# Performance work log

Measured on AMD Instinct MI355X. Metric: run time of the kernel, lower is better.

Reference implementation:

```python
import jax, jax.numpy as jnp
import numpy as np


def setup_inputs() -> dict:
    key = jax.random.key(0)
    k1, k2 = jax.random.split(key)
    B, C, T = 64, 16, 32768
    y_pred = jax.random.normal(k1, (B, C, T), dtype=jnp.float32)
    y_true = jax.random.normal(k2, (B, C, T), dtype=jnp.float32)
    return {"y_pred": y_pred, "y_true": y_true}


def reference(y_pred, y_true):
    # Original: for i in 1..T, sum |cumsum(pred[:,:,:i]) - cumsum(true[:,:,:i])|, mean over batch.
    # Prefix position t (0-indexed) appears in all outer iterations i >= t+1, i.e. (T - t) times.
    # => total = mean_b sum_{c,t} |cumsum(pred - true)[b,c,t]| * (T - t)
    B, C, T = y_pred.shape
    c = jnp.cumsum(y_pred - y_true, axis=2)          # (B, C, T)
    w = (T - jnp.arange(T)).astype(y_pred.dtype)     # weight T-t for position t
    total = jnp.sum(jnp.abs(c) * w, axis=(1, 2))     # (B,)
    total = jnp.mean(total)
    scaling = 2.0 / (T * C * (T * C + 1))            # apply_scaling_factor=True
    return scaling * total
```

## Files before the change

kernel.cpp:

```cpp
#include <hip/hip_runtime.h>

#define B_BATCH 64
#define C_CH    16
#define T_LEN   32768
#define THREADS 256
#define VEC     4
#define CHUNK   (THREADS * VEC)
#define NCHUNK  (T_LEN / CHUNK)
#define CPP     8
#define NPH     (NCHUNK / CPP)
#define PHEL    (CPP * CHUNK)
#define NROWS   (B_BATCH * C_CH)

__global__ __launch_bounds__(THREADS, 4) void wloss_scan_kernel(
    const float* __restrict__ pred,
    const float* __restrict__ tru,
    double* __restrict__ partials)
{
    __shared__ float  s_pref[PHEL];
    __shared__ float  s_wt[CPP * 4];
    __shared__ float  s_rowc;
    __shared__ double s_d[4];

    const int row  = blockIdx.x;
    const int tid  = threadIdx.x;
    const int lane = tid & 63;
    const int wave = tid >> 6;

    const float4* p4 = (const float4*)(pred + (size_t)row * T_LEN);
    const float4* t4 = (const float4*)(tru  + (size_t)row * T_LEN);

    if (tid == 0) s_rowc = 0.0f;
    double acc = 0.0;

    for (int ph = 0; ph < NPH; ++ph) {
        if (ph) __syncthreads();

        #pragma unroll
        for (int c8 = 0; c8 < CPP; ++c8) {
            const int c   = ph * CPP + c8;
            const int idx = c * (CHUNK / VEC) + tid;
            float4 p = p4[idx];
            float4 t = t4[idx];
            float d0 = p.x - t.x, d1 = p.y - t.y, d2 = p.z - t.z, d3 = p.w - t.w;
            float s1 = d0, s2 = s1 + d1, s3 = s2 + d2, s4 = s3 + d3;

            float v = s4;
            #pragma unroll
            for (int off = 1; off < 64; off <<= 1) {
                float u = __shfl_up(v, off, 64);
                if (lane >= off) v += u;
            }
            const float we = v - s4;
            float4 st = { we + s1, we + s2, we + s3, we + s4 };
            *(float4*)&s_pref[c8 * CHUNK + tid * VEC] = st;
            if (lane == 63) s_wt[c8 * 4 + wave] = v;
        }
        __syncthreads();

        if (wave == 0) {
            float val = (lane < 32) ? s_wt[lane] : 0.0f;
            float inc = val;
            #pragma unroll
            for (int off = 1; off < 32; off <<= 1) {
                float u = __shfl_up(inc, off, 64);
                if (lane >= off) inc += u;
            }
            const float rc = s_rowc;
            if (lane < 32) s_wt[lane] = rc + inc - val;
            if (lane == 31) s_rowc = rc + inc;
        }
        __syncthreads();

        #pragma unroll
        for (int c8 = 0; c8 < CPP; ++c8) {
            const float carry = s_wt[c8 * 4 + wave];
            float4 pr = *(const float4*)&s_pref[c8 * CHUNK + tid * VEC];
            const int   e0 = (ph * CPP + c8) * CHUNK + tid * VEC;
            const float w0 = (float)(T_LEN - e0);
            float part = fabsf(carry + pr.x) * w0
                       + fabsf(carry + pr.y) * (w0 - 1.0f)
                       + fabsf(carry + pr.z) * (w0 - 2.0f)
                       + fabsf(carry + pr.w) * (w0 - 3.0f);
            acc += (double)part;
        }
    }

    #pragma unroll
    for (int off = 32; off > 0; off >>= 1)
        acc += __shfl_down(acc, off, 64);
    if (lane == 0) s_d[wave] = acc;
    __syncthreads();

    if (tid == 0)
        partials[row] = s_d[0] + s_d[1] + s_d[2] + s_d[3];
}

__global__ __launch_bounds__(THREADS) void wloss_finalize_kernel(
    const double* __restrict__ partials, float* __restrict__ out)
{
    const int tid  = threadIdx.x;
    const int lane = tid & 63;
    const int wave = tid >> 6;

    double acc = 0.0;
    for (int i = tid; i < NROWS; i += THREADS) acc += partials[i];

    #pragma unroll
    for (int off = 32; off > 0; off >>= 1)
        acc += __shfl_down(acc, off, 64);

    __shared__ double dtot[4];
    if (lane == 0) dtot[wave] = acc;
    __syncthreads();

    if (tid == 0) {
        const double tot     = dtot[0] + dtot[1] + dtot[2] + dtot[3];
        const double tc      = (double)T_LEN * (double)C_CH;
        const double scaling = 2.0 / (tc * (tc + 1.0));
        out[0] = (float)(tot * scaling / (double)B_BATCH);
    }
}

extern "C" void kernel_launch(void* const* d_in, const int* in_sizes, int n_in,
                              void* d_out, int out_size, void* d_ws, size_t ws_size,
                              hipStream_t stream)
{
    const float* pred = (const float*)d_in[0];
    const float* tru  = (const float*)d_in[1];
    double*      partials = (double*)d_ws;
    float*       out      = (float*)d_out;

    wloss_scan_kernel<<<NROWS, THREADS, 0, stream>>>(pred, tru, partials);
    wloss_finalize_kernel<<<1, THREADS, 0, stream>>>(partials, out);
}
```

Baseline: 279.8 us.

## Split row scan into tile-sum and weighted-scan kernels for more parallelism

Replaces the one-block-per-row sequential chunk scan with a reduce-then-scan scheme. A first kernel computes per-tile sums of pred-true across 16 tiles per row. A second kernel computes each tile's carry from the preceding tile sums and does a local scan and weighted abs-sum. This raises the block count from 1024 to 16384 and removes the LDS-staged phases, at the cost of reading both inputs twice and adding a kernel launch.

```diff
diff --git a/kernel.cpp b/kernel.cpp
--- a/kernel.cpp
+++ b/kernel.cpp
@@ -4,96 +4,110 @@
 #define C_CH    16
 #define T_LEN   32768
 #define THREADS 256
-#define VEC     4
-#define CHUNK   (THREADS * VEC)
-#define NCHUNK  (T_LEN / CHUNK)
-#define CPP     8
-#define NPH     (NCHUNK / CPP)
-#define PHEL    (CPP * CHUNK)
+#define TPT     8
+#define TILE    (THREADS * TPT)
+#define NTILE   (T_LEN / TILE)
 #define NROWS   (B_BATCH * C_CH)
+#define NBLK    (NROWS * NTILE)
 
-__global__ __launch_bounds__(THREADS, 4) void wloss_scan_kernel(
+#define TS_OFF   0
+#define PART_OFF (NBLK * 4)
+
+__global__ __launch_bounds__(THREADS, 8) void wloss_sum_kernel(
     const float* __restrict__ pred,
     const float* __restrict__ tru,
-    double* __restrict__ partials)
+    float* __restrict__ tilesum)
 {
-    __shared__ float  s_pref[PHEL];
-    __shared__ float  s_wt[CPP * 4];
-    __shared__ float  s_rowc;
-    __shared__ double s_d[4];
-
-    const int row  = blockIdx.x;
     const int tid  = threadIdx.x;
     const int lane = tid & 63;
     const int wave = tid >> 6;
+    const int row  = blockIdx.x >> 4;
+    const int g    = blockIdx.x & (NTILE - 1);
 
-    const float4* p4 = (const float4*)(pred + (size_t)row * T_LEN);
-    const float4* t4 = (const float4*)(tru  + (size_t)row * T_LEN);
+    const size_t base = (size_t)row * T_LEN + (size_t)g * TILE;
+    const float4* p4 = (const float4*)(pred + base) + tid * 2;
+    const float4* t4 = (const float4*)(tru  + base) + tid * 2;
 
-    if (tid == 0) s_rowc = 0.0f;
-    double acc = 0.0;
+    float4 a0 = p4[0], a1 = p4[1];
+    float4 b0 = t4[0], b1 = t4[1];
 
-    for (int ph = 0; ph < NPH; ++ph) {
-        if (ph) __syncthreads();
-
-        #pragma unroll
-        for (int c8 = 0; c8 < CPP; ++c8) {
-            const int c   = ph * CPP + c8;
-            const int idx = c * (CHUNK / VEC) + tid;
-            float4 p = p4[idx];
-            float4 t = t4[idx];
-            float d0 = p.x - t.x, d1 = p.y - t.y, d2 = p.z - t.z, d3 = p.w - t.w;
-            float s1 = d0, s2 = s1 + d1, s3 = s2 + d2, s4 = s3 + d3;
-
-            float v = s4;
-            #pragma unroll
-            for (int off = 1; off < 64; off <<= 1) {
-                float u = __shfl_up(v, off, 64);
-                if (lane >= off) v += u;
-            }
-            const float we = v - s4;
-            float4 st = { we + s1, we + s2, we + s3, we + s4 };
-            *(float4*)&s_pref[c8 * CHUNK + tid * VEC] = st;
-            if (lane == 63) s_wt[c8 * 4 + wave] = v;
-        }
-        __syncthreads();
-
-        if (wave == 0) {
-            float val = (lane < 32) ? s_wt[lane] : 0.0f;
-            float inc = val;
-            #pragma unroll
-            for (int off = 1; off < 32; off <<= 1) {
-                float u = __shfl_up(inc, off, 64);
-                if (lane >= off) inc += u;
-            }
-            const float rc = s_rowc;
-            if (lane < 32) s_wt[lane] = rc + inc - val;
-            if (lane == 31) s_rowc = rc + inc;
-        }
-        __syncthreads();
-
-        #pragma unroll
-        for (int c8 = 0; c8 < CPP; ++c8) {
-            const float carry = s_wt[c8 * 4 + wave];
-            float4 pr = *(const float4*)&s_pref[c8 * CHUNK + tid * VEC];
-            const int   e0 = (ph * CPP + c8) * CHUNK + tid * VEC;
-            const float w0 = (float)(T_LEN - e0);
-            float part = fabsf(carry + pr.x) * w0
-                       + fabsf(carry + pr.y) * (w0 - 1.0f)
-                       + fabsf(carry + pr.z) * (w0 - 2.0f)
-                       + fabsf(carry + pr.w) * (w0 - 3.0f);
-            acc += (double)part;
-        }
-    }
+    float s = (a0.x - b0.x) + (a0.y - b0.y) + (a0.z - b0.z) + (a0.w - b0.w)
+            + (a1.x - b1.x) + (a1.y - b1.y) + (a1.z - b1.z) + (a1.w - b1.w);
 
     #pragma unroll
     for (int off = 32; off > 0; off >>= 1)
+        s += __shfl_down(s, off, 64);
+
+    __shared__ float s_w[4];
+    if (lane == 0) s_w[wave] = s;
+    __syncthreads();
+    if (tid == 0)
+        tilesum[blockIdx.x] = s_w[0] + s_w[1] + s_w[2] + s_w[3];
+}
+
+__global__ __launch_bounds__(THREADS, 8) void wloss_weight_kernel(
+    const float* __restrict__ pred,
+    const float* __restrict__ tru,
+    const float* __restrict__ tilesum,
+    double* __restrict__ partials)
+{
+    const int tid  = threadIdx.x;
+    const int lane = tid & 63;
+    const int wave = tid >> 6;
+    const int row  = blockIdx.x >> 4;
+    const int g    = blockIdx.x & (NTILE - 1);
+
+    const size_t base = (size_t)row * T_LEN + (size_t)g * TILE;
+    const float4* p4 = (const float4*)(pred + base) + tid * 2;
+    const float4* t4 = (const float4*)(tru  + base) + tid * 2;
+
+    float4 a0 = p4[0], a1 = p4[1];
+    float4 b0 = t4[0], b1 = t4[1];
+
+    float carry = 0.0f;
+    for (int j = 0; j < g; ++j)
+        carry += tilesum[(row << 4) + j];
+
+    float d[TPT];
+    d[0] = a0.x - b0.x; d[1] = a0.y - b0.y; d[2] = a0.z - b0.z; d[3] = a0.w - b0.w;
+    d[4] = a1.x - b1.x; d[5] = a1.y - b1.y; d[6] = a1.z - b1.z; d[7] = a1.w - b1.w;
+    #pragma unroll
+    for (int j = 1; j < TPT; ++j) d[j] += d[j-1];
+
+    float v = d[TPT-1];
+    #pragma unroll
+    for (int off = 1; off < 64; off <<= 1) {
+        float u = __shfl_up(v, off, 64);
+        if (lane >= off) v += u;
+    }
+    const float texcl = v - d[TPT-1];
+
+    __shared__ float s_w[4];
+    if (lane == 63) s_w[wave] = v;
+    __syncthreads();
+    float wprefix = 0.0f;
+    #pragma unroll
+    for (int w = 0; w < 4; ++w)
+        if (w < wave) wprefix += s_w[w];
+
+    const float excl = carry + wprefix + texcl;
+    const int   e0   = g * TILE + tid * TPT;
+    const float w0   = (float)(T_LEN - e0);
+    float part = 0.0f;
+    #pragma unroll
+    for (int j = 0; j < TPT; ++j)
+        part += fabsf(excl + d[j]) * (w0 - (float)j);
+
+    double acc = (double)part;
+    #pragma unroll
+    for (int off = 32; off > 0; off >>= 1)
         acc += __shfl_down(acc, off, 64);
+
+    __shared__ double s_d[4];
     if (lane == 0) s_d[wave] = acc;
     __syncthreads();
-
     if (tid == 0)
-        partials[row] = s_d[0] + s_d[1] + s_d[2] + s_d[3];
+        partials[blockIdx.x] = s_d[0] + s_d[1] + s_d[2] + s_d[3];
 }
 
 __global__ __launch_bounds__(THREADS) void wloss_finalize_kernel(
@@ -104,7 +118,7 @@
     const int wave = tid >> 6;
 
     double acc = 0.0;
-    for (int i = tid; i < NROWS; i += THREADS) acc += partials[i];
+    for (int i = tid; i < NBLK; i += THREADS) acc += partials[i];
 
     #pragma unroll
     for (int off = 32; off > 0; off >>= 1)
@@ -128,9 +142,11 @@
 {
     const float* pred = (const float*)d_in[0];
     const float* tru  = (const float*)d_in[1];
-    double*      partials = (double*)d_ws;
-    float*       out      = (float*)d_out;
+    float*  tilesum  = (float*) ((char*)d_ws + TS_OFF);
+    double* partials = (double*)((char*)d_ws + PART_OFF);
+    float*  out      = (float*)d_out;
 
-    wloss_scan_kernel<<<NROWS, THREADS, 0, stream>>>(pred, tru, partials);
-    wloss_finalize_kernel<<<1, THREADS, 0, stream>>>(partials, out);
+    wloss_sum_kernel     <<<NBLK, THREADS, 0, stream>>>(pred, tru, tilesum);
+    wloss_weight_kernel  <<<NBLK, THREADS, 0, stream>>>(pred, tru, tilesum, partials);
+    wloss_finalize_kernel<<<1,    THREADS, 0, stream>>>(partials, out);
 }
```

Result: slower. 322.4 us (+15.2%).

## Replace phased LDS prefix buffering with per-chunk register scan and prefetch

Applied to the files above, without the earlier changes.

The scan kernel no longer buffers eight chunks of prefixes in shared memory. Each chunk is now scanned in registers, with a double-buffered per-wave total array and a redundant cross-wave prefix computed by every thread. The next chunk's loads are issued before the current chunk is processed, and blocks grow to 512 threads. This removes about 32KB of LDS per block and the serial wave-0 scan, which should raise occupancy and overlap memory with compute. The cost is one barrier per chunk instead of three per eight chunks.

```diff
diff --git a/kernel.cpp b/kernel.cpp
--- a/kernel.cpp
+++ b/kernel.cpp
@@ -3,24 +3,20 @@
 #define B_BATCH 64
 #define C_CH    16
 #define T_LEN   32768
-#define THREADS 256
+#define THREADS 512
+#define NWAVE   (THREADS / 64)
 #define VEC     4
 #define CHUNK   (THREADS * VEC)
 #define NCHUNK  (T_LEN / CHUNK)
-#define CPP     8
-#define NPH     (NCHUNK / CPP)
-#define PHEL    (CPP * CHUNK)
 #define NROWS   (B_BATCH * C_CH)
 
-__global__ __launch_bounds__(THREADS, 4) void wloss_scan_kernel(
+__global__ __launch_bounds__(THREADS, 8) void wloss_scan_kernel(
     const float* __restrict__ pred,
     const float* __restrict__ tru,
     double* __restrict__ partials)
 {
-    __shared__ float  s_pref[PHEL];
-    __shared__ float  s_wt[CPP * 4];
-    __shared__ float  s_rowc;
-    __shared__ double s_d[4];
+    __shared__ float  s_wt[2][NWAVE];
+    __shared__ double s_d[NWAVE];
 
     const int row  = blockIdx.x;
     const int tid  = threadIdx.x;
@@ -30,60 +26,52 @@
     const float4* p4 = (const float4*)(pred + (size_t)row * T_LEN);
     const float4* t4 = (const float4*)(tru  + (size_t)row * T_LEN);
 
-    if (tid == 0) s_rowc = 0.0f;
-    double acc = 0.0;
+    float  carry = 0.0f;
+    double acc   = 0.0;
 
-    for (int ph = 0; ph < NPH; ++ph) {
-        if (ph) __syncthreads();
+    float4 cp = p4[tid];
+    float4 ct = t4[tid];
 
+    for (int ch = 0; ch < NCHUNK; ++ch) {
+        const int nx = (ch + 1 < NCHUNK ? ch + 1 : NCHUNK - 1) * (CHUNK / VEC) + tid;
+        float4 np = p4[nx];
+        float4 nt = t4[nx];
+
+        float s1 = cp.x - ct.x;
+        float s2 = s1 + (cp.y - ct.y);
+        float s3 = s2 + (cp.z - ct.z);
+        float s4 = s3 + (cp.w - ct.w);
+
+        float v = s4;
         #pragma unroll
-        for (int c8 = 0; c8 < CPP; ++c8) {
-            const int c   = ph * CPP + c8;
-            const int idx = c * (CHUNK / VEC) + tid;
-            float4 p = p4[idx];
-            float4 t = t4[idx];
-            float d0 = p.x - t.x, d1 = p.y - t.y, d2 = p.z - t.z, d3 = p.w - t.w;
-            float s1 = d0, s2 = s1 + d1, s3 = s2 + d2, s4 = s3 + d3;
+        for (int off = 1; off < 64; off <<= 1) {
+            float u = __shfl_up(v, off, 64);
+            if (lane >= off) v += u;
+        }
 
-            float v = s4;
-            #pragma unroll
-            for (int off = 1; off < 64; off <<= 1) {
-                float u = __shfl_up(v, off, 64);
-                if (lane >= off) v += u;
-            }
-            const float we = v - s4;
-            float4 st = { we + s1, we + s2, we + s3, we + s4 };
-            *(float4*)&s_pref[c8 * CHUNK + tid * VEC] = st;
-            if (lane == 63) s_wt[c8 * 4 + wave] = v;
-        }
+        const int par = ch & 1;
+        if (lane == 63) s_wt[par][wave] = v;
         __syncthreads();
 
-        if (wave == 0) {
-            float val = (lane < 32) ? s_wt[lane] : 0.0f;
-            float inc = val;
-            #pragma unroll
-            for (int off = 1; off < 32; off <<= 1) {
-                float u = __shfl_up(inc, off, 64);
-                if (lane >= off) inc += u;
-            }
-            const float rc = s_rowc;
-            if (lane < 32) s_wt[lane] = rc + inc - val;
-            if (lane == 31) s_rowc = rc + inc;
+        float wpre = 0.0f, tot = 0.0f;
+        #pragma unroll
+        for (int w = 0; w < NWAVE; ++w) {
+            float wt = s_wt[par][w];
+            if (w < wave) wpre += wt;
+            tot += wt;
         }
-        __syncthreads();
 
-        #pragma unroll
-        for (int c8 = 0; c8 < CPP; ++c8) {
-            const float carry = s_wt[c8 * 4 + wave];
-            float4 pr = *(const float4*)&s_pref[c8 * CHUNK + tid * VEC];
-            const int   e0 = (ph * CPP + c8) * CHUNK + tid * VEC;
-            const float w0 = (float)(T_LEN - e0);
-            float part = fabsf(carry + pr.x) * w0
-                       + fabsf(carry + pr.y) * (w0 - 1.0f)
-                       + fabsf(carry + pr.z) * (w0 - 2.0f)
-                       + fabsf(carry + pr.w) * (w0 - 3.0f);
-            acc += (double)part;
-        }
+        const float excl = carry + wpre + (v - s4);
+        const int   e0   = ch * CHUNK + tid * VEC;
+        const float w0   = (float)(T_LEN - e0);
+        float part = fabsf(excl + s1) *  w0
+                   + fabsf(excl + s2) * (w0 - 1.0f)
+                   + fabsf(excl + s3) * (w0 - 2.0f)
+                   + fabsf(excl + s4) * (w0 - 3.0f);
+        acc   += (double)part;
+        carry += tot;
+
+        cp = np; ct = nt;
     }
 
     #pragma unroll
@@ -92,11 +80,15 @@
     if (lane == 0) s_d[wave] = acc;
     __syncthreads();
 
-    if (tid == 0)
-        partials[row] = s_d[0] + s_d[1] + s_d[2] + s_d[3];
+    if (tid == 0) {
+        double s = 0.0;
+        #pragma unroll
+        for (int w = 0; w < NWAVE; ++w) s += s_d[w];
+        partials[row] = s;
+    }
 }
 
-__global__ __launch_bounds__(THREADS) void wloss_finalize_kernel(
+__global__ __launch_bounds__(256) void wloss_finalize_kernel(
     const double* __restrict__ partials, float* __restrict__ out)
 {
     const int tid  = threadIdx.x;
@@ -104,7 +96,7 @@
     const int wave = tid >> 6;
 
     double acc = 0.0;
-    for (int i = tid; i < NROWS; i += THREADS) acc += partials[i];
+    for (int i = tid; i < NROWS; i += 256) acc += partials[i];
 
     #pragma unroll
     for (int off = 32; off > 0; off >>= 1)
@@ -128,9 +120,9 @@
 {
     const float* pred = (const float*)d_in[0];
     const float* tru  = (const float*)d_in[1];
-    double*      partials = (double*)d_ws;
-    float*       out      = (float*)d_out;
+    double* partials  = (double*)d_ws;
+    float*  out       = (float*)d_out;
 
-    wloss_scan_kernel<<<NROWS, THREADS, 0, stream>>>(pred, tru, partials);
-    wloss_finalize_kernel<<<1, THREADS, 0, stream>>>(partials, out);
+    wloss_scan_kernel    <<<NROWS, THREADS, 0, stream>>>(pred, tru, partials);
+    wloss_finalize_kernel<<<1,     256,     0, stream>>>(partials, out);
 }
```

Measured after the change: 280.3 us. Within noise of the previous version (+0.2%).
